# Kernel optimization log

Measured on AMD Instinct MI355X. Metric: run time of the kernel, lower is better.

The kernel has to match this reference:

```python
import jax, jax.numpy as jnp
import numpy as np

UNITS = 300
MDN_MIXES = 8  # Config.mdn_mixes: 3*8=24 MDN params + 1 length = 25-dim feedback
FEAT = 25
GATE_IN = 2 * FEAT  # concat(inputs, prev_output)


def setup_inputs() -> dict:
    key = jax.random.key(0)
    ks = jax.random.split(key, 12)
    B, T = 2048, 512
    x = jax.random.uniform(ks[0], (B, T, FEAT), dtype=jnp.float32)
    s = 0.05
    kernel = jax.random.normal(ks[1], (FEAT, 4 * UNITS), dtype=jnp.float32) * s
    recurrent_kernel = jax.random.normal(ks[2], (UNITS, 4 * UNITS), dtype=jnp.float32) * s
    # unit_forget_bias: zeros except forget-gate slice = ones
    bias = jnp.concatenate([
        jnp.zeros((UNITS,), jnp.float32),
        jnp.ones((UNITS,), jnp.float32),
        jnp.zeros((2 * UNITS,), jnp.float32),
    ])
    # MLPGate: 2-layer MLP combining the two 25-dim distributions -> 24-dim
    mlp_w1 = jax.random.normal(ks[3], (GATE_IN, GATE_IN), dtype=jnp.float32) * s
    mlp_b1 = jnp.zeros((GATE_IN,), jnp.float32)
    mlp_w2 = jax.random.normal(ks[4], (GATE_IN, FEAT - 1), dtype=jnp.float32) * s
    mlp_b2 = jnp.zeros((FEAT - 1,), jnp.float32)
    # MDN heads on h (units -> mdn_mixes each)
    wa = jax.random.normal(ks[5], (UNITS, MDN_MIXES), dtype=jnp.float32) * s
    ba = jnp.zeros((MDN_MIXES,), jnp.float32)
    wm = jax.random.normal(ks[6], (UNITS, MDN_MIXES), dtype=jnp.float32) * s
    bm = jnp.zeros((MDN_MIXES,), jnp.float32)
    ws = jax.random.normal(ks[7], (UNITS, MDN_MIXES), dtype=jnp.float32) * s
    bs = jnp.zeros((MDN_MIXES,), jnp.float32)
    return {
        'x': x, 'kernel': kernel, 'recurrent_kernel': recurrent_kernel, 'bias': bias,
        'mlp_w1': mlp_w1, 'mlp_b1': mlp_b1, 'mlp_w2': mlp_w2, 'mlp_b2': mlp_b2,
        'wa': wa, 'ba': ba, 'wm': wm, 'bm': bm, 'ws': ws, 'bs': bs,
    }


def _hard_sigmoid(z):
    return jnp.clip(0.2 * z + 0.5, 0.0, 1.0)


def _nnelu(z):
    return 1.0 + jax.nn.elu(z)


def reference(x, kernel, recurrent_kernel, bias,
              mlp_w1, mlp_b1, mlp_w2, mlp_b2,
              wa, ba, wm, bm, ws, bs):
    B = x.shape[0]
    dt = x.dtype

    def step(carry, xt):
        h, c, prev = carry  # [B,U], [B,U], [B,25]
        il = xt[:, 24:25]
        pl = prev[:, 24:25]
        combined = il + pl
        denom = jnp.maximum(combined, jnp.asarray(1e-8, dt))  # LengthNormalizer
        inp2 = jnp.concatenate([xt[:, :24], il / denom], axis=1)
        prev2 = jnp.concatenate([prev[:, :24], pl / denom], axis=1)
        # MLP gate combining the two distributions
        g = jax.nn.relu(jnp.concatenate([inp2, prev2], axis=1) @ mlp_w1 + mlp_b1)
        g = g @ mlp_w2 + mlp_b2  # [B,24]
        gate_out = jnp.concatenate([g, combined], axis=1)  # [B,25]
        # LSTM gates (split-kernel math == fused without dropout)
        z = gate_out @ kernel + h @ recurrent_kernel + bias  # [B,4U]
        zi, zf, zc, zo = jnp.split(z, 4, axis=1)
        i = _hard_sigmoid(zi)
        f = _hard_sigmoid(zf)
        o = _hard_sigmoid(zo)
        c_new = f * c + i * jnp.tanh(zc)
        h_new = o * jnp.tanh(c_new)
        # MDN heads
        alpha = jax.nn.softmax(h_new @ wa + ba, axis=-1)
        mu = h_new @ wm + bm
        sigma = _nnelu(h_new @ ws + bs)
        mdn = jnp.concatenate([alpha, mu, sigma, combined], axis=1)  # [B,25]
        return (h_new, c_new, mdn), mdn

    h0 = jnp.zeros((B, UNITS), dt)
    c0 = jnp.zeros((B, UNITS), dt)
    prev0 = jnp.zeros((B, FEAT), dt)
    xt = jnp.swapaxes(x, 0, 1)  # [T,B,25]
    _, ys = jax.lax.scan(step, (h0, c0, prev0), xt)
    return jnp.swapaxes(ys, 0, 1)  # [B,T,25]
```

## Files before the change

### kernel.cpp

```cpp
#include <hip/hip_runtime.h>
#include <math.h>

#define BB 2048
#define TT 512
#define NFEAT 25
#define UNITS 300
#define RPB 16
#define NBLK (BB/RPB)
#define NT 512
#define KS12 12
#define NKS 11
#define TPW 10
#define HROW 360
#define F8ROW 392
#define GROW 72

#define OFF_M1 0
#define SZ_M1  (4*2*512)
#define OFF_H  (OFF_M1 + SZ_M1)
#define SZ_H   (2*NKS*512)
#define OFF_BZ (OFF_H + SZ_H)
#define OFF_WK (OFF_BZ + 2560)
#define OFF_F8 (OFF_WK + 2560)
#define SZ_F8B (8*KS12*TPW*512)
#define SW_SZ  (SZ_M1 + SZ_H)
#define SWM1   0
#define SWH    (SZ_M1)

typedef __attribute__((ext_vector_type(4))) float f32x4;
typedef __attribute__((ext_vector_type(8))) short bf16x8;
typedef long long ll8;

static __device__ __forceinline__ unsigned short f2bf(float f) {
    union { float f; unsigned u; } x; x.f = f;
    unsigned r = (x.u + 0x7fffu + ((x.u >> 16) & 1u)) >> 16;
    return (unsigned short)r;
}
static __device__ __forceinline__ unsigned char f2f8(float f) {
    return (unsigned char)(__builtin_amdgcn_cvt_pk_fp8_f32(f, 0.f, 0, false) & 0xff);
}
static __device__ __forceinline__ float ftanh(float v) {
    float e = __builtin_amdgcn_exp2f(v * 2.8853900817779268f);
    return 1.f - 2.f * __builtin_amdgcn_rcpf(e + 1.f);
}
static __device__ __forceinline__ int zcol(int c) { return (c & 3) * 300 + (c >> 2); }

__global__ __launch_bounds__(256) void conv_b8(
    const float* __restrict__ wk, const float* __restrict__ wr,
    const float* __restrict__ w2, unsigned char* __restrict__ dst8)
{
    int idx = blockIdx.x * 256 + threadIdx.x;
    if (idx >= SZ_F8B) return;
    int j = idx & 7, n = (idx >> 3) & 15, kg = (idx >> 7) & 3, q = idx >> 9;
    int i = q % TPW, ks = (q / TPW) % KS12, w = q / (TPW * KS12);
    int k = ks * 32 + kg * 8 + j, c = (w + 8 * i) * 16 + n;
    float v = 0.f;
    if (c < 1200) {
        int oc = zcol(c);
        if (ks < 2) {
            if (k < 50) {
                float s = 0.f;
                for (int j2 = 0; j2 < 24; ++j2)
                    s += w2[k * 24 + j2] * wk[j2 * 1200 + oc];
                v = 8.f * s;
            }
        } else {
            int u = k - 64;
            if (u < 300) v = wr[u * 1200 + oc];
        }
    }
    dst8[idx] = f2f8(v);
}

__global__ __launch_bounds__(256) void conv_misc(
    const float* __restrict__ wk, const float* __restrict__ bz,
    const float* __restrict__ b2, float* __restrict__ bzdst,
    float* __restrict__ wkdst)
{
    int i = blockIdx.x * 256 + threadIdx.x;
    if (i >= 1280) return;
    float vb = 0.f, vw = 0.f;
    if (i < 1200) {
        int oc = zcol(i);
        vb = bz[oc];
        for (int j = 0; j < 24; ++j) vb += b2[j] * wk[j * 1200 + oc];
        vw = wk[24 * 1200 + oc];
    }
    bzdst[i] = vb;
    wkdst[i] = vw;
}

__global__ __launch_bounds__(256) void conv_gen(
    const float* __restrict__ W, unsigned short* __restrict__ dst,
    int K, int N, int nks, int total)
{
    int idx = blockIdx.x * 256 + threadIdx.x;
    if (idx >= total) return;
    int j = idx & 7, n = (idx >> 3) & 15, kg = (idx >> 7) & 3, qq = idx >> 9;
    int ks = qq % nks, nt = qq / nks;
    int k = ks * 32 + kg * 8 + j, col = nt * 16 + n;
    float v = (k < K && col < N) ? W[k * N + col] : 0.f;
    dst[idx] = f2bf(v);
}

__global__ __launch_bounds__(256) void conv_heads(
    const float* __restrict__ wa, const float* __restrict__ wm,
    const float* __restrict__ wsg, unsigned short* __restrict__ dst)
{
    int idx = blockIdx.x * 256 + threadIdx.x;
    if (idx >= SZ_H) return;
    int j = idx & 7, n = (idx >> 3) & 15, kg = (idx >> 7) & 3, qq = idx >> 9;
    int ks = qq % NKS, nt = qq / NKS;
    int k = ks * 32 + kg * 8 + j, col = nt * 16 + n;
    float v = 0.f;
    if (k >= 32 && k < 332 && col < 24) {
        int u = k - 32, h = col >> 3, m = col & 7;
        const float* W = (h == 0) ? wa : (h == 1) ? wm : wsg;
        v = W[u * 8 + m];
    }
    dst[idx] = f2bf(v);
}

#define MFMA   __builtin_amdgcn_mfma_f32_16x16x32_bf16
#define MFMA8  __builtin_amdgcn_mfma_f32_16x16x32_fp8_fp8

__global__ __launch_bounds__(NT, 2)
void dilstm(
    const float* __restrict__ x,
    const unsigned short* __restrict__ wf,
    const float* __restrict__ b1v,
    const float* __restrict__ ba,
    const float* __restrict__ bm,
    const float* __restrict__ bs,
    float* __restrict__ out)
{
    __shared__ unsigned short Hbf[RPB][HROW];
    __shared__ __attribute__((aligned(16))) unsigned char Af8[RPB][F8ROW];
    __shared__ __attribute__((aligned(16))) unsigned char G1b8[RPB][64];
    __shared__ unsigned short Gbf[RPB][GROW];
    __shared__ float Sc[RPB][24];
    __shared__ float BzS[1280];
    __shared__ float WkS[1280];
    __shared__ float CombS[RPB];
    __shared__ float B1S[64];
    __shared__ float Zw[8][2][16][20];
    __shared__ unsigned short SW[SW_SZ];

    const int t = threadIdx.x;
    const int lane = t & 63, wv = t >> 6;
    const int arow = lane & 15, akg = lane >> 4;
    const int crow0 = akg * 4;
    const int u_l = lane & 3, rr = lane >> 2;
    const int row0 = blockIdx.x * RPB;

    for (int i = t; i < RPB * HROW; i += NT) ((unsigned short*)Hbf)[i] = 0;
    for (int i = t; i < RPB * F8ROW; i += NT) ((unsigned char*)Af8)[i] = 0;
    for (int i = t; i < RPB * 64; i += NT) ((unsigned char*)G1b8)[i] = 0;
    for (int i = t; i < RPB * GROW; i += NT) ((unsigned short*)Gbf)[i] = 0;
    for (int i = t; i < SW_SZ; i += NT) SW[i] = wf[OFF_M1 + i];
    {
        const float* bzp = (const float*)(wf + OFF_BZ);
        const float* wkp = (const float*)(wf + OFF_WK);
        for (int i = t; i < 1280; i += NT) { BzS[i] = bzp[i]; WkS[i] = wkp[i]; }
    }
    if (t < 64) B1S[t] = (t < 50) ? b1v[t] : 0.f;

    float hbias = 0.f;
    {
        int c1 = wv * 16 + arow;
        if (wv < 2 && c1 < 24)
            hbias = (c1 < 8) ? ba[c1] : (c1 < 16) ? bm[c1 - 8] : bs[c1 - 16];
    }

    float creg[TPW];
    #pragma unroll
    for (int i = 0; i < TPW; ++i) creg[i] = 0.f;

    const unsigned char* bw8 = (const unsigned char*)(wf + OFF_F8)
                               + (size_t)wv * (KS12 * TPW * 512) + (lane << 3);
    const unsigned char* af8p = &Af8[0][0] + arow * F8ROW + akg * 8;

    const int rA = t / 25, eA = t - (t / 25) * 25;
    float combreg = 0.f, xreg = 0.f;
    if (t < RPB * NFEAT) xreg = x[((size_t)(row0 + rA) * TT) * NFEAT + eA];
    __syncthreads();

    if (t < RPB * NFEAT) {
        if (eA < 24) {
            Gbf[rA][eA] = f2bf(xreg);
        } else {
            float comb = xreg;
            combreg = comb;
            float denom = fmaxf(comb, 1e-8f);
            Gbf[rA][24] = f2bf(xreg / denom);
            CombS[rA] = comb;
        }
    }
    __syncthreads();

    for (int ts = 0; ts < TT; ++ts) {
        f32x4 acc[TPW];
        #pragma unroll
        for (int i = 0; i < TPW; ++i) acc[i] = (f32x4){0.f, 0.f, 0.f, 0.f};

        if (wv < 4) {
            bf16x8 ga0 = *(const bf16x8*)&Gbf[arow][akg * 8];
            bf16x8 ga1 = *(const bf16x8*)&Gbf[arow][32 + akg * 8];
            bf16x8 b0 = *(const bf16x8*)&SW[SWM1 + (wv * 2 + 0) * 512 + (lane << 3)];
            bf16x8 b1 = *(const bf16x8*)&SW[SWM1 + (wv * 2 + 1) * 512 + (lane << 3)];
            f32x4 m1 = {0.f, 0.f, 0.f, 0.f};
            m1 = MFMA(ga0, b0, m1, 0, 0, 0);
            m1 = MFMA(ga1, b1, m1, 0, 0, 0);
            int col = wv * 16 + arow;
            if (col < 50) {
                #pragma unroll
                for (int rg = 0; rg < 4; ++rg)
                    G1b8[crow0 + rg][col] = f2f8(0.125f * fmaxf(m1[rg] + B1S[col], 0.f));
            }
        }

        if (t < RPB * NFEAT && ts + 1 < TT)
            xreg = x[((size_t)(row0 + rA) * TT + (ts + 1)) * NFEAT + eA];

        {
            const unsigned char* bp = bw8 + 2 * (TPW * 512);
            ll8 bbA[TPW], bbB[TPW];
            #pragma unroll
            for (int i = 0; i < TPW; ++i)
                bbA[i] = *(const ll8*)(bp + i * 512);
            #pragma unroll 1
            for (int pr = 0; pr < 5; ++pr) {
                const int ks = 2 * pr + 2;
                #pragma unroll
                for (int i = 0; i < TPW; ++i)
                    bbB[i] = *(const ll8*)(bp + 5120 + i * 512);
                ll8 a8a = *(const ll8*)(af8p + ks * 32);
                #pragma unroll
                for (int i = 0; i < TPW; ++i)
                    acc[i] = MFMA8(a8a, bbA[i], acc[i], 0, 0, 0);
                if (pr < 4) {
                    #pragma unroll
                    for (int i = 0; i < TPW; ++i)
                        bbA[i] = *(const ll8*)(bp + 10240 + i * 512);
                }
                ll8 a8b = *(const ll8*)(af8p + ks * 32 + 32);
                #pragma unroll
                for (int i = 0; i < TPW; ++i)
                    acc[i] = MFMA8(a8b, bbB[i], acc[i], 0, 0, 0);
                bp += 10240;
            }
        }
        __syncthreads();

        {
            ll8 g0 = *(const ll8*)&G1b8[arow][akg * 8];
            ll8 g1 = *(const ll8*)&G1b8[arow][32 + akg * 8];
            ll8 c0[TPW], c1[TPW];
            #pragma unroll
            for (int i = 0; i < TPW; ++i) c0[i] = *(const ll8*)(bw8 + i * 512);
            #pragma unroll
            for (int i = 0; i < TPW; ++i) c1[i] = *(const ll8*)(bw8 + 5120 + i * 512);
            #pragma unroll
            for (int i = 0; i < TPW; ++i) acc[i] = MFMA8(g0, c0[i], acc[i], 0, 0, 0);
            #pragma unroll
            for (int i = 0; i < TPW; ++i) acc[i] = MFMA8(g1, c1[i], acc[i], 0, 0, 0);

            float cmb = CombS[rr];
            *(f32x4*)&Zw[wv][0][arow][crow0] = acc[0];
            #pragma unroll
            for (int i = 0; i < TPW; ++i) {
                if (i + 1 < TPW)
                    *(f32x4*)&Zw[wv][(i + 1) & 1][arow][crow0] = acc[i + 1];
                f32x4 bz4 = *(const f32x4*)&BzS[(wv + 8 * i) * 16 + 4 * u_l];
                f32x4 wk4 = *(const f32x4*)&WkS[(wv + 8 * i) * 16 + 4 * u_l];
                const float* zp = &Zw[wv][i & 1][4 * u_l][rr];
                float zi = zp[0]  + bz4[0] + cmb * wk4[0];
                float zf = zp[20] + bz4[1] + cmb * wk4[1];
                float zc = zp[40] + bz4[2] + cmb * wk4[2];
                float zo = zp[60] + bz4[3] + cmb * wk4[3];
                if (wv + 8 * i < 75) {
                    float ig = fminf(fmaxf(0.2f * zi + 0.5f, 0.f), 1.f);
                    float fg = fminf(fmaxf(0.2f * zf + 0.5f, 0.f), 1.f);
                    float og = fminf(fmaxf(0.2f * zo + 0.5f, 0.f), 1.f);
                    float cn = fg * creg[i] + ig * ftanh(zc);
                    creg[i] = cn;
                    float hn = og * ftanh(cn);
                    int hb = (wv + 8 * i) * 4 + u_l;
                    Hbf[rr][32 + hb] = f2bf(hn);
                    Af8[rr][64 + hb] = f2f8(hn);
                }
            }
        }
        __syncthreads();

        if (wv < 2) {
            f32x4 e0 = {0.f, 0.f, 0.f, 0.f}, e1 = {0.f, 0.f, 0.f, 0.f};
            #pragma unroll
            for (int ks = 1; ks < NKS; ks += 2) {
                bf16x8 a0 = *(const bf16x8*)&Hbf[arow][ks * 32 + akg * 8];
                bf16x8 b0 = *(const bf16x8*)&SW[SWH + (wv * NKS + ks) * 512 + (lane << 3)];
                e0 = MFMA(a0, b0, e0, 0, 0, 0);
                bf16x8 a1 = *(const bf16x8*)&Hbf[arow][(ks + 1) * 32 + akg * 8];
                bf16x8 b1 = *(const bf16x8*)&SW[SWH + (wv * NKS + ks + 1) * 512 + (lane << 3)];
                e1 = MFMA(a1, b1, e1, 0, 0, 0);
            }
            int col = wv * 16 + arow;
            if (col < 24) {
                #pragma unroll
                for (int rg = 0; rg < 4; ++rg)
                    Sc[crow0 + rg][col] = e0[rg] + e1[rg] + hbias;
            }
        }
        __syncthreads();

        if (t < RPB * NFEAT) {
            float v;
            if (eA < 8) {
                float mx = Sc[rA][0];
                #pragma unroll
                for (int m = 1; m < 8; ++m) mx = fmaxf(mx, Sc[rA][m]);
                float sum = 0.f;
                #pragma unroll
                for (int m = 0; m < 8; ++m)
                    sum += __builtin_amdgcn_exp2f((Sc[rA][m] - mx) * 1.4426950408889634f);
                v = __builtin_amdgcn_exp2f((Sc[rA][eA] - mx) * 1.4426950408889634f) / sum;
            } else if (eA < 16) {
                v = Sc[rA][eA];
            } else if (eA < 24) {
                float s = Sc[rA][eA];
                v = (s > 0.f) ? (1.f + s) : __builtin_amdgcn_exp2f(s * 1.4426950408889634f);
            } else {
                v = combreg;
            }
            out[((size_t)(row0 + rA) * TT + ts) * NFEAT + eA] = v;
            if (eA < 24) {
                Gbf[rA][eA]      = f2bf(xreg);
                Gbf[rA][25 + eA] = f2bf(v);
            } else {
                float comb = xreg + combreg;
                float denom = fmaxf(comb, 1e-8f);
                Gbf[rA][24] = f2bf(xreg / denom);
                Gbf[rA][49] = f2bf(combreg / denom);
                CombS[rA] = comb;
                combreg = comb;
            }
        }
        __syncthreads();
    }
}

extern "C" void kernel_launch(void* const* d_in, const int* in_sizes, int n_in,
                              void* d_out, int out_size, void* d_ws, size_t ws_size,
                              hipStream_t stream) {
    const float* x   = (const float*)d_in[0];
    const float* wk  = (const float*)d_in[1];
    const float* wr  = (const float*)d_in[2];
    const float* bz  = (const float*)d_in[3];
    const float* w1  = (const float*)d_in[4];
    const float* b1  = (const float*)d_in[5];
    const float* w2  = (const float*)d_in[6];
    const float* b2  = (const float*)d_in[7];
    const float* wa  = (const float*)d_in[8];
    const float* ba  = (const float*)d_in[9];
    const float* wm  = (const float*)d_in[10];
    const float* bm  = (const float*)d_in[11];
    const float* wsg = (const float*)d_in[12];
    const float* bs  = (const float*)d_in[13];
    float* out = (float*)d_out;
    unsigned short* wf = (unsigned short*)d_ws;
    unsigned char*  wf8 = (unsigned char*)(wf + OFF_F8);
    float* bzdst = (float*)(wf + OFF_BZ);
    float* wkdst = (float*)(wf + OFF_WK);

    conv_b8<<<(SZ_F8B + 255) / 256, 256, 0, stream>>>(wk, wr, w2, wf8);
    conv_misc<<<(1280 + 255) / 256, 256, 0, stream>>>(wk, bz, b2, bzdst, wkdst);
    conv_gen<<<(SZ_M1 + 255) / 256, 256, 0, stream>>>(w1, wf + OFF_M1, 50, 50, 2, SZ_M1);
    conv_heads<<<(SZ_H + 255) / 256, 256, 0, stream>>>(wa, wm, wsg, wf + OFF_H);
    dilstm<<<NBLK, NT, 0, stream>>>(x, wf, b1, ba, bm, bs, out);
}
```

Baseline: 4.320 ms.

## Specialize wave 0 for MDN/MLP work and drop to two barriers per step

Restructures the per-step schedule. Wave 0 now handles the MDN head, the softmax/output writes, the MLP gate and x prefetch serially, and takes only 3 LSTM column tiles. The other 7 waves each take 11 tiles, using a new contiguous tile layout for the fp8 weights. This removes two of the four block-wide barriers per timestep by pipelining the MDN output of step t-1 into the start of step t. The cost is load imbalance: wave 0 does a long serial chain while the other waves carry more MFMA tiles and use more registers.

```diff
diff --git a/kernel.cpp b/kernel.cpp
--- a/kernel.cpp
+++ b/kernel.cpp
@@ -4,13 +4,10 @@
 #define BB 2048
 #define TT 512
 #define NFEAT 25
-#define UNITS 300
 #define RPB 16
 #define NBLK (BB/RPB)
 #define NT 512
-#define KS12 12
 #define NKS 11
-#define TPW 10
 #define HROW 360
 #define F8ROW 392
 #define GROW 72
@@ -22,7 +19,7 @@
 #define OFF_BZ (OFF_H + SZ_H)
 #define OFF_WK (OFF_BZ + 2560)
 #define OFF_F8 (OFF_WK + 2560)
-#define SZ_F8B (8*KS12*TPW*512)
+#define SZ_F8B (12*80*512)
 #define SW_SZ  (SZ_M1 + SZ_H)
 #define SWM1   0
 #define SWH    (SZ_M1)
@@ -52,8 +49,8 @@
     int idx = blockIdx.x * 256 + threadIdx.x;
     if (idx >= SZ_F8B) return;
     int j = idx & 7, n = (idx >> 3) & 15, kg = (idx >> 7) & 3, q = idx >> 9;
-    int i = q % TPW, ks = (q / TPW) % KS12, w = q / (TPW * KS12);
-    int k = ks * 32 + kg * 8 + j, c = (w + 8 * i) * 16 + n;
+    int tile = q % 80, ks = q / 80;
+    int k = ks * 32 + kg * 8 + j, c = tile * 16 + n;
     float v = 0.f;
     if (c < 1200) {
         int oc = zcol(c);
@@ -66,7 +63,7 @@
             }
         } else {
             int u = k - 64;
-            if (u < 300) v = wr[u * 1200 + oc];
+            if (u >= 0 && u < 300) v = wr[u * 1200 + oc];
         }
     }
     dst8[idx] = f2f8(v);
@@ -123,6 +120,79 @@
 
 #define MFMA   __builtin_amdgcn_mfma_f32_16x16x32_bf16
 #define MFMA8  __builtin_amdgcn_mfma_f32_16x16x32_fp8_fp8
+#define LOG2E  1.4426950408889634f
+
+#define HGEMM(NTILE) do {                                                     \
+    const unsigned char* bp_ = bw8 + (size_t)(160 + toff) * 512;              \
+    ll8 bbA[NTILE], bbB[NTILE];                                               \
+    _Pragma("unroll")                                                         \
+    for (int i = 0; i < NTILE; ++i) bbA[i] = *(const ll8*)(bp_ + i * 512);    \
+    _Pragma("unroll 1")                                                       \
+    for (int pr = 0; pr < 5; ++pr) {                                          \
+        const int ks = 2 * pr + 2;                                            \
+        _Pragma("unroll")                                                     \
+        for (int i = 0; i < NTILE; ++i)                                       \
+            bbB[i] = *(const ll8*)(bp_ + 40960 + i * 512);                    \
+        ll8 a8a = *(const ll8*)(af8p + ks * 32);                              \
+        _Pragma("unroll")                                                     \
+        for (int i = 0; i < NTILE; ++i)                                       \
+            acc[i] = MFMA8(a8a, bbA[i], acc[i], 0, 0, 0);                     \
+        if (pr < 4) {                                                         \
+            _Pragma("unroll")                                                 \
+            for (int i = 0; i < NTILE; ++i)                                   \
+                bbA[i] = *(const ll8*)(bp_ + 81920 + i * 512);                \
+        }                                                                     \
+        ll8 a8b = *(const ll8*)(af8p + ks * 32 + 32);                         \
+        _Pragma("unroll")                                                     \
+        for (int i = 0; i < NTILE; ++i)                                       \
+            acc[i] = MFMA8(a8b, bbB[i], acc[i], 0, 0, 0);                     \
+        bp_ += 81920;                                                         \
+    }                                                                         \
+} while (0)
+
+#define GCELL(NTILE) do {                                                     \
+    ll8 g0 = *(const ll8*)&G1b8[arow][akg * 8];                               \
+    ll8 g1 = *(const ll8*)&G1b8[arow][32 + akg * 8];                          \
+    {                                                                         \
+        ll8 c0[NTILE], c1[NTILE];                                             \
+        _Pragma("unroll")                                                     \
+        for (int i = 0; i < NTILE; ++i)                                       \
+            c0[i] = *(const ll8*)(bw8 + (size_t)(toff + i) * 512);            \
+        _Pragma("unroll")                                                     \
+        for (int i = 0; i < NTILE; ++i)                                       \
+            c1[i] = *(const ll8*)(bw8 + (size_t)(80 + toff + i) * 512);       \
+        _Pragma("unroll")                                                     \
+        for (int i = 0; i < NTILE; ++i) acc[i] = MFMA8(g0, c0[i], acc[i],0,0,0); \
+        _Pragma("unroll")                                                     \
+        for (int i = 0; i < NTILE; ++i) acc[i] = MFMA8(g1, c1[i], acc[i],0,0,0); \
+    }                                                                         \
+    float cmb = CombS[rr];                                                    \
+    *(f32x4*)&Zw[wv][0][arow][crow0] = acc[0];                                \
+    _Pragma("unroll")                                                         \
+    for (int i = 0; i < NTILE; ++i) {                                         \
+        if (i + 1 < NTILE)                                                    \
+            *(f32x4*)&Zw[wv][(i + 1) & 1][arow][crow0] = acc[i + 1];          \
+        int gt = toff + i;                                                    \
+        f32x4 bz4 = *(const f32x4*)&BzS[gt * 16 + 4 * u_l];                   \
+        f32x4 wk4 = *(const f32x4*)&WkS[gt * 16 + 4 * u_l];                   \
+        const float* zp = &Zw[wv][i & 1][4 * u_l][rr];                        \
+        float zi = zp[0]  + bz4[0] + cmb * wk4[0];                            \
+        float zf = zp[20] + bz4[1] + cmb * wk4[1];                            \
+        float zc = zp[40] + bz4[2] + cmb * wk4[2];                            \
+        float zo = zp[60] + bz4[3] + cmb * wk4[3];                            \
+        if (gt < 75) {                                                        \
+            float ig = fminf(fmaxf(0.2f * zi + 0.5f, 0.f), 1.f);              \
+            float fg = fminf(fmaxf(0.2f * zf + 0.5f, 0.f), 1.f);              \
+            float og = fminf(fmaxf(0.2f * zo + 0.5f, 0.f), 1.f);              \
+            float cn = fg * creg[i] + ig * ftanh(zc);                         \
+            creg[i] = cn;                                                     \
+            float hn = og * ftanh(cn);                                        \
+            int hb = gt * 4 + u_l;                                            \
+            Hbf[rr][32 + hb] = f2bf(hn);                                      \
+            Af8[rr][64 + hb] = f2f8(hn);                                      \
+        }                                                                     \
+    }                                                                         \
+} while (0)
 
 __global__ __launch_bounds__(NT, 2)
 void dilstm(
@@ -152,6 +222,7 @@
     const int crow0 = akg * 4;
     const int u_l = lane & 3, rr = lane >> 2;
     const int row0 = blockIdx.x * RPB;
+    const int toff = (wv == 0) ? 0 : 3 + 11 * (wv - 1);
 
     for (int i = t; i < RPB * HROW; i += NT) ((unsigned short*)Hbf)[i] = 0;
     for (int i = t; i < RPB * F8ROW; i += NT) ((unsigned char*)Af8)[i] = 0;
@@ -165,185 +236,148 @@
     }
     if (t < 64) B1S[t] = (t < 50) ? b1v[t] : 0.f;
 
-    float hbias = 0.f;
-    {
-        int c1 = wv * 16 + arow;
-        if (wv < 2 && c1 < 24)
-            hbias = (c1 < 8) ? ba[c1] : (c1 < 16) ? bm[c1 - 8] : bs[c1 - 16];
-    }
-
-    float creg[TPW];
+    float hb0 = 0.f, hb1 = 0.f;
+    if (wv == 0) {
+        int c0 = arow, c1 = 16 + arow;
+        hb0 = (c0 < 8) ? ba[c0] : bm[c0 - 8];
+        if (c1 < 24) hb1 = bs[c1 - 16];
+    }
+
+    float creg[11];
     #pragma unroll
-    for (int i = 0; i < TPW; ++i) creg[i] = 0.f;
-
-    const unsigned char* bw8 = (const unsigned char*)(wf + OFF_F8)
-                               + (size_t)wv * (KS12 * TPW * 512) + (lane << 3);
+    for (int i = 0; i < 11; ++i) creg[i] = 0.f;
+    f32x4 acc[11];
+
+    const unsigned char* bw8 = (const unsigned char*)(wf + OFF_F8) + (lane << 3);
     const unsigned char* af8p = &Af8[0][0] + arow * F8ROW + akg * 8;
 
-    const int rA = t / 25, eA = t - (t / 25) * 25;
-    float combreg = 0.f, xreg = 0.f;
-    if (t < RPB * NFEAT) xreg = x[((size_t)(row0 + rA) * TT) * NFEAT + eA];
+    float xr[7];
+    if (wv == 0) {
+        #pragma unroll
+        for (int k = 0; k < 7; ++k) {
+            int idx = 64 * k + lane;
+            xr[k] = (idx < 400)
+                ? x[((size_t)(row0 + idx / 25) * TT) * NFEAT + idx % 25] : 0.f;
+        }
+    }
     __syncthreads();
 
-    if (t < RPB * NFEAT) {
-        if (eA < 24) {
-            Gbf[rA][eA] = f2bf(xreg);
-        } else {
-            float comb = xreg;
-            combreg = comb;
-            float denom = fmaxf(comb, 1e-8f);
-            Gbf[rA][24] = f2bf(xreg / denom);
-            CombS[rA] = comb;
-        }
-    }
-    __syncthreads();
-
-    for (int ts = 0; ts < TT; ++ts) {
-        f32x4 acc[TPW];
+    if (wv == 0) {
         #pragma unroll
-        for (int i = 0; i < TPW; ++i) acc[i] = (f32x4){0.f, 0.f, 0.f, 0.f};
-
-        if (wv < 4) {
-            bf16x8 ga0 = *(const bf16x8*)&Gbf[arow][akg * 8];
-            bf16x8 ga1 = *(const bf16x8*)&Gbf[arow][32 + akg * 8];
-            bf16x8 b0 = *(const bf16x8*)&SW[SWM1 + (wv * 2 + 0) * 512 + (lane << 3)];
-            bf16x8 b1 = *(const bf16x8*)&SW[SWM1 + (wv * 2 + 1) * 512 + (lane << 3)];
-            f32x4 m1 = {0.f, 0.f, 0.f, 0.f};
-            m1 = MFMA(ga0, b0, m1, 0, 0, 0);
-            m1 = MFMA(ga1, b1, m1, 0, 0, 0);
-            int col = wv * 16 + arow;
-            if (col < 50) {
-                #pragma unroll
-                for (int rg = 0; rg < 4; ++rg)
-                    G1b8[crow0 + rg][col] = f2f8(0.125f * fmaxf(m1[rg] + B1S[col], 0.f));
-            }
-        }
-
-        if (t < RPB * NFEAT && ts + 1 < TT)
-            xreg = x[((size_t)(row0 + rA) * TT + (ts + 1)) * NFEAT + eA];
-
-        {
-            const unsigned char* bp = bw8 + 2 * (TPW * 512);
-            ll8 bbA[TPW], bbB[TPW];
-            #pragma unroll
-            for (int i = 0; i < TPW; ++i)
-                bbA[i] = *(const ll8*)(bp + i * 512);
-            #pragma unroll 1
-            for (int pr = 0; pr < 5; ++pr) {
-                const int ks = 2 * pr + 2;
-                #pragma unroll
-                for (int i = 0; i < TPW; ++i)
-                    bbB[i] = *(const ll8*)(bp + 5120 + i * 512);
-                ll8 a8a = *(const ll8*)(af8p + ks * 32);
-                #pragma unroll
-                for (int i = 0; i < TPW; ++i)
-                    acc[i] = MFMA8(a8a, bbA[i], acc[i], 0, 0, 0);
-                if (pr < 4) {
-                    #pragma unroll
-                    for (int i = 0; i < TPW; ++i)
-                        bbA[i] = *(const ll8*)(bp + 10240 + i * 512);
-                }
-                ll8 a8b = *(const ll8*)(af8p + ks * 32 + 32);
-                #pragma unroll
-                for (int i = 0; i < TPW; ++i)
-                    acc[i] = MFMA8(a8b, bbB[i], acc[i], 0, 0, 0);
-                bp += 10240;
-            }
-        }
-        __syncthreads();
-
-        {
-            ll8 g0 = *(const ll8*)&G1b8[arow][akg * 8];
-            ll8 g1 = *(const ll8*)&G1b8[arow][32 + akg * 8];
-            ll8 c0[TPW], c1[TPW];
-            #pragma unroll
-            for (int i = 0; i < TPW; ++i) c0[i] = *(const ll8*)(bw8 + i * 512);
-            #pragma unroll
-            for (int i = 0; i < TPW; ++i) c1[i] = *(const ll8*)(bw8 + 5120 + i * 512);
-            #pragma unroll
-            for (int i = 0; i < TPW; ++i) acc[i] = MFMA8(g0, c0[i], acc[i], 0, 0, 0);
-            #pragma unroll
-            for (int i = 0; i < TPW; ++i) acc[i] = MFMA8(g1, c1[i], acc[i], 0, 0, 0);
-
-            float cmb = CombS[rr];
-            *(f32x4*)&Zw[wv][0][arow][crow0] = acc[0];
-            #pragma unroll
-            for (int i = 0; i < TPW; ++i) {
-                if (i + 1 < TPW)
-                    *(f32x4*)&Zw[wv][(i + 1) & 1][arow][crow0] = acc[i + 1];
-                f32x4 bz4 = *(const f32x4*)&BzS[(wv + 8 * i) * 16 + 4 * u_l];
-                f32x4 wk4 = *(const f32x4*)&WkS[(wv + 8 * i) * 16 + 4 * u_l];
-                const float* zp = &Zw[wv][i & 1][4 * u_l][rr];
-                float zi = zp[0]  + bz4[0] + cmb * wk4[0];
-                float zf = zp[20] + bz4[1] + cmb * wk4[1];
-                float zc = zp[40] + bz4[2] + cmb * wk4[2];
-                float zo = zp[60] + bz4[3] + cmb * wk4[3];
-                if (wv + 8 * i < 75) {
-                    float ig = fminf(fmaxf(0.2f * zi + 0.5f, 0.f), 1.f);
-                    float fg = fminf(fmaxf(0.2f * zf + 0.5f, 0.f), 1.f);
-                    float og = fminf(fmaxf(0.2f * zo + 0.5f, 0.f), 1.f);
-                    float cn = fg * creg[i] + ig * ftanh(zc);
-                    creg[i] = cn;
-                    float hn = og * ftanh(cn);
-                    int hb = (wv + 8 * i) * 4 + u_l;
-                    Hbf[rr][32 + hb] = f2bf(hn);
-                    Af8[rr][64 + hb] = f2f8(hn);
+        for (int k = 0; k < 7; ++k) {
+            int idx = 64 * k + lane;
+            if (idx < 400) {
+                int row = idx / 25, e = idx - row * 25;
+                if (e < 24) {
+                    Gbf[row][e] = f2bf(xr[k]);
+                } else {
+                    float comb = xr[k];
+                    float denom = fmaxf(comb, 1e-8f);
+                    Gbf[row][24] = f2bf(xr[k] / denom);
+                    CombS[row] = comb;
                 }
             }
         }
-        __syncthreads();
-
-        if (wv < 2) {
-            f32x4 e0 = {0.f, 0.f, 0.f, 0.f}, e1 = {0.f, 0.f, 0.f, 0.f};
+    }
+
+    for (int ts = 0; ts <= TT; ++ts) {
+        if (wv == 0) {
+            if (ts > 0) {
+                #pragma unroll
+                for (int ct = 0; ct < 2; ++ct) {
+                    f32x4 e0 = {0.f,0.f,0.f,0.f}, e1 = {0.f,0.f,0.f,0.f};
+                    #pragma unroll
+                    for (int ks = 1; ks < NKS; ks += 2) {
+                        bf16x8 a0 = *(const bf16x8*)&Hbf[arow][ks * 32 + akg * 8];
+                        bf16x8 b0 = *(const bf16x8*)&SW[SWH + (ct * NKS + ks) * 512 + (lane << 3)];
+                        e0 = MFMA(a0, b0, e0, 0, 0, 0);
+                        bf16x8 a1 = *(const bf16x8*)&Hbf[arow][(ks + 1) * 32 + akg * 8];
+                        bf16x8 b1 = *(const bf16x8*)&SW[SWH + (ct * NKS + ks + 1) * 512 + (lane << 3)];
+                        e1 = MFMA(a1, b1, e1, 0, 0, 0);
+                    }
+                    int col = ct * 16 + arow;
+                    float hbv = ct ? hb1 : hb0;
+                    if (col < 24) {
+                        #pragma unroll
+                        for (int rg = 0; rg < 4; ++rg)
+                            Sc[crow0 + rg][col] = e0[rg] + e1[rg] + hbv;
+                    }
+                }
+                #pragma unroll
+                for (int k = 0; k < 7; ++k) {
+                    int idx = 64 * k + lane;
+                    if (idx < 400) {
+                        int row = idx / 25, e = idx - row * 25;
+                        float v;
+                        if (e < 8) {
+                            float mx = Sc[row][0];
+                            #pragma unroll
+                            for (int m = 1; m < 8; ++m) mx = fmaxf(mx, Sc[row][m]);
+                            float sum = 0.f;
+                            #pragma unroll
+                            for (int m = 0; m < 8; ++m)
+                                sum += __builtin_amdgcn_exp2f((Sc[row][m] - mx) * LOG2E);
+                            v = __builtin_amdgcn_exp2f((Sc[row][e] - mx) * LOG2E) / sum;
+                        } else if (e < 16) {
+                            v = Sc[row][e];
+                        } else if (e < 24) {
+                            float s = Sc[row][e];
+                            v = (s > 0.f) ? (1.f + s) : __builtin_amdgcn_exp2f(s * LOG2E);
+                        } else {
+                            v = CombS[row];
+                        }
+                        out[((size_t)(row0 + row) * TT + (ts - 1)) * NFEAT + e] = v;
+                        if (e < 24) {
+                            Gbf[row][e]      = f2bf(xr[k]);
+                            Gbf[row][25 + e] = f2bf(v);
+                        } else {
+                            float comb = xr[k] + v;
+                            float denom = fmaxf(comb, 1e-8f);
+                            Gbf[row][24] = f2bf(xr[k] / denom);
+                            Gbf[row][49] = f2bf(v / denom);
+                            CombS[row] = comb;
+                        }
+                    }
+                }
+            }
+            if (ts < TT) {
+                bf16x8 ga0 = *(const bf16x8*)&Gbf[arow][akg * 8];
+                bf16x8 ga1 = *(const bf16x8*)&Gbf[arow][32 + akg * 8];
+                #pragma unroll
+                for (int ct = 0; ct < 4; ++ct) {
+                    bf16x8 b0 = *(const bf16x8*)&SW[SWM1 + (ct * 2 + 0) * 512 + (lane << 3)];
+                    bf16x8 b1 = *(const bf16x8*)&SW[SWM1 + (ct * 2 + 1) * 512 + (lane << 3)];
+                    f32x4 m1 = {0.f, 0.f, 0.f, 0.f};
+                    m1 = MFMA(ga0, b0, m1, 0, 0, 0);
+                    m1 = MFMA(ga1, b1, m1, 0, 0, 0);
+                    int col = ct * 16 + arow;
+                    if (col < 50) {
+                        #pragma unroll
+                        for (int rg = 0; rg < 4; ++rg)
+                            G1b8[crow0 + rg][col] = f2f8(0.125f * fmaxf(m1[rg] + B1S[col], 0.f));
+                    }
+                }
+                if (ts + 1 < TT) {
+                    #pragma unroll
+                    for (int k = 0; k < 7; ++k) {
+                        int idx = 64 * k + lane;
+                        if (idx < 400)
+                            xr[k] = x[((size_t)(row0 + idx / 25) * TT + ts + 1) * NFEAT + idx % 25];
+                    }
+                }
+                #pragma unroll
+                for (int i = 0; i < 3; ++i) acc[i] = (f32x4){0.f, 0.f, 0.f, 0.f};
+                HGEMM(3);
+            }
+        } else if (ts < TT) {
             #pragma unroll
-            for (int ks = 1; ks < NKS; ks += 2) {
-                bf16x8 a0 = *(const bf16x8*)&Hbf[arow][ks * 32 + akg * 8];
-                bf16x8 b0 = *(const bf16x8*)&SW[SWH + (wv * NKS + ks) * 512 + (lane << 3)];
-                e0 = MFMA(a0, b0, e0, 0, 0, 0);
-                bf16x8 a1 = *(const bf16x8*)&Hbf[arow][(ks + 1) * 32 + akg * 8];
-                bf16x8 b1 = *(const bf16x8*)&SW[SWH + (wv * NKS + ks + 1) * 512 + (lane << 3)];
-                e1 = MFMA(a1, b1, e1, 0, 0, 0);
-            }
-            int col = wv * 16 + arow;
-            if (col < 24) {
-                #pragma unroll
-                for (int rg = 0; rg < 4; ++rg)
-                    Sc[crow0 + rg][col] = e0[rg] + e1[rg] + hbias;
-            }
+            for (int i = 0; i < 11; ++i) acc[i] = (f32x4){0.f, 0.f, 0.f, 0.f};
+            HGEMM(11);
         }
         __syncthreads();
 
-        if (t < RPB * NFEAT) {
-            float v;
-            if (eA < 8) {
-                float mx = Sc[rA][0];
-                #pragma unroll
-                for (int m = 1; m < 8; ++m) mx = fmaxf(mx, Sc[rA][m]);
-                float sum = 0.f;
-                #pragma unroll
-                for (int m = 0; m < 8; ++m)
-                    sum += __builtin_amdgcn_exp2f((Sc[rA][m] - mx) * 1.4426950408889634f);
-                v = __builtin_amdgcn_exp2f((Sc[rA][eA] - mx) * 1.4426950408889634f) / sum;
-            } else if (eA < 16) {
-                v = Sc[rA][eA];
-            } else if (eA < 24) {
-                float s = Sc[rA][eA];
-                v = (s > 0.f) ? (1.f + s) : __builtin_amdgcn_exp2f(s * 1.4426950408889634f);
-            } else {
-                v = combreg;
-            }
-            out[((size_t)(row0 + rA) * TT + ts) * NFEAT + eA] = v;
-            if (eA < 24) {
-                Gbf[rA][eA]      = f2bf(xreg);
-                Gbf[rA][25 + eA] = f2bf(v);
-            } else {
-                float comb = xreg + combreg;
-                float denom = fmaxf(comb, 1e-8f);
-                Gbf[rA][24] = f2bf(xreg / denom);
-                Gbf[rA][49] = f2bf(combreg / denom);
-                CombS[rA] = comb;
-                combreg = comb;
-            }
+        if (ts < TT) {
+            if (wv == 0) { GCELL(3); } else { GCELL(11); }
         }
         __syncthreads();
     }
```

Result: slower. 7.461 ms (+72.7%).
